# Kernel tuning notes

Measured on AMD Instinct MI355X. Metric: run time of the kernel, lower is better.

The kernel has to match this reference:

```python
import jax, jax.numpy as jnp
import numpy as np

M, N, P, T = 8000, 63, 64, 5


def setup_inputs() -> dict:
    key = jax.random.key(0)
    ks = jax.random.split(key, 19)
    sn = (1.0 / N) ** 0.5
    sp = (1.0 / P) ** 0.5
    f32 = jnp.float32
    return {
        "A": jax.random.normal(ks[0], (1, M, N), f32),
        "b": jax.random.normal(ks[1], (1, M), f32),
        "c": jax.random.normal(ks[2], (1, N), f32),
        "theta1r": sn * jax.random.normal(ks[3], (P, N + 1), f32),
        "theta1c": sn * jax.random.normal(ks[4], (P, N + 1), f32),
        "theta2rr": sp * jax.random.normal(ks[5], (P, P), f32),
        "theta2rc": sp * jax.random.normal(ks[6], (P, P), f32),
        "theta2cr": sp * jax.random.normal(ks[7], (P, P), f32),
        "theta3rr": sp * jax.random.normal(ks[8], (P, P), f32),
        "theta3rc": sp * jax.random.normal(ks[9], (P, P), f32),
        "theta3cr": sp * jax.random.normal(ks[10], (P, P), f32),
        "theta4rr": sp * jax.random.normal(ks[11], (P,), f32),
        "theta4rc": sp * jax.random.normal(ks[12], (P,), f32),
        "theta4cr": sp * jax.random.normal(ks[13], (P,), f32),
        "theta6r": sp * jax.random.normal(ks[14], (P, P), f32),
        "theta6c": sp * jax.random.normal(ks[15], (P, P), f32),
        "theta7": sp * jax.random.normal(ks[16], (P, P), f32),
        "W8": 0.05 * jax.random.normal(ks[17], (2, 2 * P), f32),
        "b8": 0.05 * jax.random.normal(ks[18], (2,), f32),
        "z": 7,
    }


def reference(A, b, c, theta1r, theta1c, theta2rr, theta2rc, theta2cr,
              theta3rr, theta3rc, theta3cr, theta4rr, theta4rc, theta4cr,
              theta6r, theta6c, theta7, W8, b8, z):
    relu = jax.nn.relu
    m, n = A.shape[1], A.shape[2]
    p = theta1r.shape[0]
    # raw node features: row node v -> [A[v,:], b[v]]; column node m -> [c, 0]
    Fr_raw = jnp.concatenate([A[0], b[0][:, None]], axis=1)        # (m, n+1)
    fc_raw = jnp.concatenate([c[0], jnp.zeros((1,), A.dtype)])     # (n+1,)
    Fr = Fr_raw / jnp.linalg.norm(Fr_raw, axis=1, keepdims=True)   # f(v), v < m
    fc = fc_raw / jnp.linalg.norm(fc_raw)                          # f(m)
    # edge weights w(v,u) = f(v).f(u) are detached in the original (float(...data))
    Frd = jax.lax.stop_gradient(Fr)
    fcd = jax.lax.stop_gradient(fc)
    Wrr = Frd @ Frd.T                                              # (m, m)
    dg = jnp.diagonal(Wrr)
    srr_pos = relu(Wrr).sum(axis=1) - relu(dg)                     # sum over u != v
    srr_neg = relu(-Wrr).sum(axis=1) - relu(-dg)
    wrc = Frd @ fcd                                                # (m,) = w(v, m)
    # identity: sum_u relu(t4 * w_u) = relu(t4) * sum_u relu(w_u) + relu(-t4) * sum_u relu(-w_u)
    Srr = relu(theta4rr)[:, None] * srr_pos[None, :] + relu(-theta4rr)[:, None] * srr_neg[None, :]
    Src = relu(theta4rc)[:, None] * relu(wrc)[None, :] + relu(-theta4rc)[:, None] * relu(-wrc)[None, :]
    scr = relu(theta4cr) * relu(wrc).sum() + relu(-theta4cr) * relu(-wrc).sum()
    edge_r = theta3rr @ Srr + theta3rc @ Src                       # (p, m), constant over t
    edge_c = theta3cr @ scr                                        # (p,)
    fz = Fr[z]                                                     # z < m: row node feature
    t1r = theta1r @ fz                                             # (p,)
    t1c = theta1c @ fz
    # mu init (p, m+1) = [[Ab^T, c0^T]; 0]; split into row columns / column node
    mu_r0 = jnp.zeros((p, m), A.dtype).at[: n + 1].set(Fr_raw.T)
    mu_c0 = jnp.zeros((p,), A.dtype).at[: n + 1].set(fc_raw)

    def step(carry, _):
        mu_r, mu_c = carry
        # row nodes: term2rr uses old mu[:, v]; term2rc uses old mu[:, m]
        new_r = relu(t1r[:, None] + theta2rr @ mu_r + (theta2rc @ mu_c)[:, None] + edge_r)
        # column node updated last within a sweep -> sees updated row embeddings
        new_c = relu(t1c + theta2cr @ new_r.sum(axis=1) + edge_c)
        return (new_r, new_c), None

    (mu_r, mu_c), _ = jax.lax.scan(step, (mu_r0, mu_c0), None, length=T)
    term6 = theta6r @ mu_r.sum(axis=1) + theta6c @ mu_c            # (p,)
    term7 = theta7 @ mu_r[:, z]                                    # (p,)
    feat = jax.nn.sigmoid(jnp.concatenate([term6, term7]))         # (2p,)
    return (feat @ W8.T + b8)[None, :]                             # (1, 2)
```

## Files before the change

### kernel.cpp

```cpp
#include <hip/hip_runtime.h>
#include <math.h>

typedef __attribute__((ext_vector_type(8))) short short8;
typedef __attribute__((ext_vector_type(4))) float f32x4;

#define WS_SPART 0
#define WS_GPART 262144
#define WS_WPART 270336
#define WS_CPART 270592
#define WS_T1R   310592
#define WS_T1C   310656
#define WS_AL    310720
#define WS_BE    310784
#define WS_GA    310848
#define WS_DE    310912
#define WS_ECP   310976
#define WS_ECN   311040
#define WS_W     311104
#define WS_MUZ   311168
#define WS_WSUM  311232
#define WS_RNORM 311296
#define WS_R2H   319488
#define WS_R2L   321536
#define WS_E4    323584
#define WS_FH    355584
#define WS_FL    617728

__device__ __forceinline__ float waveReduceSum(float v) {
#pragma unroll
    for (int m = 32; m >= 1; m >>= 1) v += __shfl_xor(v, m, 64);
    return v;
}
__device__ __forceinline__ unsigned short f2bf(float f) {
    unsigned int u = __float_as_uint(f);
    unsigned int r = (u + 0x7fffu + ((u >> 16) & 1u)) >> 16;
    return (unsigned short)r;
}
__device__ __forceinline__ float bf2f(unsigned short h) {
    return __uint_as_float(((unsigned int)h) << 16);
}

__global__ __launch_bounds__(256) void k_fr(
    const float* __restrict__ A, const float* __restrict__ b, const float* __restrict__ c,
    const float* __restrict__ th1r, const float* __restrict__ th1c,
    const float* __restrict__ th2rr, const float* __restrict__ th2rc,
    const float* __restrict__ th3rr, const float* __restrict__ th3rc, const float* __restrict__ th3cr,
    const float* __restrict__ th4rr, const float* __restrict__ th4rc, const float* __restrict__ th4cr,
    const int* __restrict__ zp,
    unsigned short* __restrict__ Fh, unsigned short* __restrict__ Fl,
    unsigned short* __restrict__ R2H, unsigned short* __restrict__ R2L,
    float* __restrict__ ws)
{
    int tid = threadIdx.x, lane = tid & 63, wid = tid >> 6;

    if (blockIdx.x == 128) {
        __shared__ float fcraw[64], fz[64], sh4a[64], sh4b[64];
        int p = lane;
        int z = zp[0];
        float cv = (p < 63) ? c[p] : 0.f;
        fcraw[p] = cv;
        float av = (p < 63) ? A[z * 63 + p] : b[z];
        float s2 = waveReduceSum(av * av);
        fz[p] = av * rsqrtf(s2);
        __syncthreads();

        float t1 = 0.f, t2 = 0.f, w0 = 0.f;
#pragma unroll 8
        for (int k = 0; k < 64; k++) {
            t1 += th1r[p * 64 + k] * fz[k];
            t2 += th1c[p * 64 + k] * fz[k];
            w0 += th2rc[p * 64 + k] * fcraw[k];
        }
        ws[WS_T1R + p] = t1;
        ws[WS_T1C + p] = t2;
        ws[WS_W + p] = t1 + w0;

        sh4a[p] = th4rr[p];
        sh4b[p] = th4rc[p];
        __syncthreads();
        float a = 0.f, bb = 0.f, g = 0.f, d = 0.f;
#pragma unroll 8
        for (int k = 0; k < 64; k++) {
            float t4 = sh4a[k];
            a  += th3rr[p * 64 + k] * fmaxf(t4, 0.f);
            bb += th3rr[p * 64 + k] * fmaxf(-t4, 0.f);
            float t5 = sh4b[k];
            g  += th3rc[p * 64 + k] * fmaxf(t5, 0.f);
            d  += th3rc[p * 64 + k] * fmaxf(-t5, 0.f);
        }
        ws[WS_AL + p] = a; ws[WS_BE + p] = bb;
        ws[WS_GA + p] = g; ws[WS_DE + p] = d;
        __syncthreads();
        sh4a[p] = th4cr[p];
        __syncthreads();
        float e1 = 0.f, e2 = 0.f;
#pragma unroll 8
        for (int k = 0; k < 64; k++) {
            float t6 = sh4a[k];
            e1 += th3cr[p * 64 + k] * fmaxf(t6, 0.f);
            e2 += th3cr[p * 64 + k] * fmaxf(-t6, 0.f);
        }
        ws[WS_ECP + p] = e1; ws[WS_ECN + p] = e2;

#pragma unroll
        for (int i = 0; i < 16; i++) {
            int idx = tid * 16 + i;
            float f = th2rr[idx];
            unsigned short h = f2bf(f);
            R2H[idx] = h;
            R2L[idx] = f2bf(f - bf2f(h));
        }
        return;
    }

    __shared__ float gsh[64];
    __shared__ float wsh2[2];
    if (tid < 64) gsh[tid] = 0.f;
    if (tid < 2) wsh2[tid] = 0.f;
    __syncthreads();

    float cv = (lane < 63) ? c[lane] : 0.f;
    float cn2 = waveReduceSum(cv * cv);
    float fcnl = cv * rsqrtf(cn2);

    int gw = blockIdx.x * 4 + wid;
    float gl = 0.f, lp = 0.f, ln = 0.f;
    for (int r = gw; r < 8192; r += 512) {
        if (r < 8000) {
            float val = (lane < 63) ? A[r * 63 + lane] : b[r];
            float s2 = waveReduceSum(val * val);
            float f = val * rsqrtf(s2);
            unsigned short h = f2bf(f);
            Fh[r * 64 + lane] = h;
            Fl[r * 64 + lane] = f2bf(f - bf2f(h));
            gl += f;
            float w = waveReduceSum(f * fcnl);
            if (lane == 0) {
                ws[WS_RNORM + r] = sqrtf(s2);
                lp += fmaxf(w, 0.f); ln += fmaxf(-w, 0.f);
            }
        } else {
            Fh[r * 64 + lane] = 0;
            Fl[r * 64 + lane] = 0;
        }
    }
    atomicAdd(&gsh[lane], gl);
    if (lane == 0) { atomicAdd(&wsh2[0], lp); atomicAdd(&wsh2[1], ln); }
    __syncthreads();
    if (tid < 64) ws[WS_GPART + blockIdx.x * 64 + tid] = gsh[tid];
    if (tid == 64) ws[WS_WPART + blockIdx.x * 2 + 0] = wsh2[0];
    if (tid == 65) ws[WS_WPART + blockIdx.x * 2 + 1] = wsh2[1];
}

__global__ __launch_bounds__(256) void k_gram(
    const unsigned short* __restrict__ Fh, const unsigned short* __restrict__ Fl,
    float* __restrict__ ws)
{
    int tid = threadIdx.x, lane = tid & 63, wid = tid >> 6;
    int m = lane & 15, quad = lane >> 4;
    int vbase = blockIdx.x * 256 + wid * 64;

    short8 AH[8], AL[8];
#pragma unroll
    for (int pt = 0; pt < 4; pt++)
#pragma unroll
        for (int q = 0; q < 2; q++) {
            int off = (vbase + pt * 16 + m) * 64 + q * 32 + quad * 8;
            AH[pt * 2 + q] = *(const short8*)(Fh + off);
            AL[pt * 2 + q] = *(const short8*)(Fl + off);
        }
    float srr[16];
#pragma unroll
    for (int i = 0; i < 16; i++) srr[i] = 0.f;

    const int y = blockIdx.y;
    const int boff = m * 64 + quad * 8;
    short8 B0h[2], B0l[2], B1h[2], B1l[2];
#pragma unroll
    for (int q = 0; q < 2; q++) {
        B0h[q] = *(const short8*)(Fh + y * 16 * 64 + boff + q * 32);
        B0l[q] = *(const short8*)(Fl + y * 16 * 64 + boff + q * 32);
    }
#pragma unroll 1
    for (int ii = 0; ii < 8; ii++) {
        int tB1 = y + 64 * ii + 32;
#pragma unroll
        for (int q = 0; q < 2; q++) {
            B1h[q] = *(const short8*)(Fh + tB1 * 16 * 64 + boff + q * 32);
            B1l[q] = *(const short8*)(Fl + tB1 * 16 * 64 + boff + q * 32);
        }
#pragma unroll
        for (int pt = 0; pt < 4; pt++) {
            f32x4 a = {0.f, 0.f, 0.f, 0.f};
#pragma unroll
            for (int q = 0; q < 2; q++) {
                a = __builtin_amdgcn_mfma_f32_16x16x32_bf16(AH[pt*2+q], B0h[q], a, 0, 0, 0);
                a = __builtin_amdgcn_mfma_f32_16x16x32_bf16(AH[pt*2+q], B0l[q], a, 0, 0, 0);
                a = __builtin_amdgcn_mfma_f32_16x16x32_bf16(AL[pt*2+q], B0h[q], a, 0, 0, 0);
            }
#pragma unroll
            for (int r = 0; r < 4; r++) srr[pt*4+r] += fmaxf(a[r], 0.f);
        }
        if (ii < 7) {
            int tB0 = y + 64 * ii + 64;
#pragma unroll
            for (int q = 0; q < 2; q++) {
                B0h[q] = *(const short8*)(Fh + tB0 * 16 * 64 + boff + q * 32);
                B0l[q] = *(const short8*)(Fl + tB0 * 16 * 64 + boff + q * 32);
            }
        }
#pragma unroll
        for (int pt = 0; pt < 4; pt++) {
            f32x4 a = {0.f, 0.f, 0.f, 0.f};
#pragma unroll
            for (int q = 0; q < 2; q++) {
                a = __builtin_amdgcn_mfma_f32_16x16x32_bf16(AH[pt*2+q], B1h[q], a, 0, 0, 0);
                a = __builtin_amdgcn_mfma_f32_16x16x32_bf16(AH[pt*2+q], B1l[q], a, 0, 0, 0);
                a = __builtin_amdgcn_mfma_f32_16x16x32_bf16(AL[pt*2+q], B1h[q], a, 0, 0, 0);
            }
#pragma unroll
            for (int r = 0; r < 4; r++) srr[pt*4+r] += fmaxf(a[r], 0.f);
        }
    }
#pragma unroll
    for (int pt = 0; pt < 4; pt++)
#pragma unroll
        for (int r = 0; r < 4; r++) {
            float s = srr[pt * 4 + r];
#pragma unroll
            for (int mm = 8; mm >= 1; mm >>= 1) s += __shfl_xor(s, mm, 64);
            if (m == 0)
                ws[WS_SPART + y * 8192 + vbase + pt * 16 + quad * 4 + r] = s;
        }
}

__global__ __launch_bounds__(256) void k_e4(
    const float* __restrict__ c, float* __restrict__ ws,
    unsigned short* __restrict__ MH, unsigned short* __restrict__ ML)
{
    __shared__ float fcnS[64], gS[64], sprow[64], red[256];
    int tid = threadIdx.x, lane = tid & 63, wid = tid >> 6;

    float cv = (lane < 63) ? c[lane] : 0.f;
    float cn2 = waveReduceSum(cv * cv);
    if (wid == 0) fcnS[lane] = cv * rsqrtf(cn2);

    float gv = 0.f;
#pragma unroll 8
    for (int blk = wid * 32; blk < wid * 32 + 32; blk++)
        gv += ws[WS_GPART + blk * 64 + lane];
    red[tid] = gv;
    __syncthreads();
    if (tid < 64) gS[tid] = red[tid] + red[64 + tid] + red[128 + tid] + red[192 + tid];
    if (wid == 1) {
        float wp = ws[WS_WPART + lane * 2] + ws[WS_WPART + (lane + 64) * 2];
        wp = waveReduceSum(wp);
        if (lane == 0) ws[WS_WSUM] = wp;
    }
    if (wid == 2) {
        float wn = ws[WS_WPART + lane * 2 + 1] + ws[WS_WPART + (lane + 64) * 2 + 1];
        wn = waveReduceSum(wn);
        if (lane == 0) ws[WS_WSUM + 1] = wn;
    }
    int v0 = blockIdx.x * 64;
    float sv = 0.f;
#pragma unroll
    for (int y = wid * 8; y < wid * 8 + 8; y++)
        sv += ws[WS_SPART + y * 8192 + v0 + lane];
    __syncthreads();
    red[tid] = sv;
    __syncthreads();
    if (tid < 64) sprow[tid] = red[tid] + red[64 + tid] + red[128 + tid] + red[192 + tid];
    __syncthreads();

    for (int i2 = 0; i2 < 16; i2++) {
        int i = wid * 16 + i2;
        int v = v0 + i;
        unsigned short fh = MH[v * 64 + lane];
        unsigned short fl = ML[v * 64 + lane];
        float fr = bf2f(fh) + bf2f(fl);
        float dw = waveReduceSum(fr * fcnS[lane]);
        float dg = waveReduceSum(fr * gS[lane]);
        if (lane == 0) {
            float spv = sprow[i];
            float4 e;
            e.x = spv - 1.0f;
            e.y = spv - dg;
            e.z = fmaxf(dw, 0.f);
            e.w = fmaxf(-dw, 0.f);
            *(float4*)(ws + WS_E4 + v * 4) = e;
        }
        float rnv = ws[WS_RNORM + v];
        float x = fr * rnv;
        unsigned short h = f2bf(x);
        MH[v * 64 + lane] = h;
        ML[v * 64 + lane] = f2bf(x - bf2f(h));
    }
}

__global__ __launch_bounds__(256) void k_iter(
    const float* __restrict__ th2cr, const float* __restrict__ th2rc,
    const int* __restrict__ zp, float* __restrict__ ws,
    unsigned short* __restrict__ MH, unsigned short* __restrict__ ML,
    const unsigned short* __restrict__ R2H, const unsigned short* __restrict__ R2L,
    int t)
{
    __shared__ __align__(16) float wsh[64], alS[64], beS[64], gaS[64], deS[64];
    __shared__ float red[256], Ssh[64], ysh[64], colp[256];
    int tid = threadIdx.x, lane = tid & 63, wid = tid >> 6;
    int m = lane & 15, quad = lane >> 4;
    int v = (blockIdx.x * 4 + wid) * 16 + m;

    if (tid < 64) {
        alS[tid] = ws[WS_AL + tid]; beS[tid] = ws[WS_BE + tid];
        gaS[tid] = ws[WS_GA + tid]; deS[tid] = ws[WS_DE + tid];
    }
    if (t == 0) {
        if (tid >= 64 && tid < 128) wsh[tid - 64] = ws[WS_W + tid - 64];
        __syncthreads();
    } else {
        float s = 0.f;
        for (int blk = wid; blk < 125; blk += 4)
            s += ws[WS_CPART + (t - 1) * 8000 + blk * 64 + lane];
        red[tid] = s;
        __syncthreads();
        if (tid < 64) Ssh[tid] = red[tid] + red[64 + tid] + red[128 + tid] + red[192 + tid];
        __syncthreads();
        {
            int p = wid * 16 + m;
            float acc = 0.f;
            const float4* rowp = (const float4*)(th2cr + p * 64 + quad * 16);
#pragma unroll
            for (int kk = 0; kk < 4; kk++) {
                float4 r4 = rowp[kk];
                acc += r4.x * Ssh[quad * 16 + 4 * kk]     + r4.y * Ssh[quad * 16 + 4 * kk + 1]
                     + r4.z * Ssh[quad * 16 + 4 * kk + 2] + r4.w * Ssh[quad * 16 + 4 * kk + 3];
            }
            acc += __shfl_xor(acc, 16, 64);
            acc += __shfl_xor(acc, 32, 64);
            if (quad == 0)
                ysh[p] = fmaxf(acc + ws[WS_T1C + p] + ws[WS_WSUM] * ws[WS_ECP + p]
                               + ws[WS_WSUM + 1] * ws[WS_ECN + p], 0.f);
        }
        __syncthreads();
        {
            int p = wid * 16 + m;
            float acc = 0.f;
            const float4* rowp = (const float4*)(th2rc + p * 64 + quad * 16);
#pragma unroll
            for (int kk = 0; kk < 4; kk++) {
                float4 r4 = rowp[kk];
                acc += r4.x * ysh[quad * 16 + 4 * kk]     + r4.y * ysh[quad * 16 + 4 * kk + 1]
                     + r4.z * ysh[quad * 16 + 4 * kk + 2] + r4.w * ysh[quad * 16 + 4 * kk + 3];
            }
            acc += __shfl_xor(acc, 16, 64);
            acc += __shfl_xor(acc, 32, 64);
            if (quad == 0) wsh[p] = acc + ws[WS_T1R + p];
        }
        __syncthreads();
    }

    short8 RH[8], RL[8];
#pragma unroll
    for (int pt = 0; pt < 4; pt++)
#pragma unroll
        for (int q = 0; q < 2; q++) {
            int off = (pt * 16 + m) * 64 + q * 32 + quad * 8;
            RH[pt * 2 + q] = *(const short8*)(R2H + off);
            RL[pt * 2 + q] = *(const short8*)(R2L + off);
        }
    short8 BH[2], BL[2];
#pragma unroll
    for (int q = 0; q < 2; q++) {
        BH[q] = *(const short8*)(MH + v * 64 + q * 32 + quad * 8);
        BL[q] = *(const short8*)(ML + v * 64 + q * 32 + quad * 8);
    }
    float4 e = *(const float4*)(ws + WS_E4 + v * 4);
    int z = zp[0];

#pragma unroll
    for (int pt = 0; pt < 4; pt++) {
        f32x4 a = {0.f, 0.f, 0.f, 0.f};
#pragma unroll
        for (int q = 0; q < 2; q++) {
            a = __builtin_amdgcn_mfma_f32_16x16x32_bf16(RH[pt*2+q], BH[q], a, 0, 0, 0);
            a = __builtin_amdgcn_mfma_f32_16x16x32_bf16(RH[pt*2+q], BL[q], a, 0, 0, 0);
            a = __builtin_amdgcn_mfma_f32_16x16x32_bf16(RL[pt*2+q], BH[q], a, 0, 0, 0);
        }
        int pbase = pt * 16 + quad * 4;
        float4 w4 = *(const float4*)(wsh + pbase);
        float4 a4 = *(const float4*)(alS + pbase);
        float4 b4 = *(const float4*)(beS + pbase);
        float4 g4 = *(const float4*)(gaS + pbase);
        float4 d4 = *(const float4*)(deS + pbase);
        float v0 = fmaxf(a[0] + w4.x + a4.x*e.x + b4.x*e.y + g4.x*e.z + d4.x*e.w, 0.f);
        float v1 = fmaxf(a[1] + w4.y + a4.y*e.x + b4.y*e.y + g4.y*e.z + d4.y*e.w, 0.f);
        float v2 = fmaxf(a[2] + w4.z + a4.z*e.x + b4.z*e.y + g4.z*e.z + d4.z*e.w, 0.f);
        float v3 = fmaxf(a[3] + w4.w + a4.w*e.x + b4.w*e.y + g4.w*e.z + d4.w*e.w, 0.f);
        ushort4 h4, l4;
        h4.x = f2bf(v0); l4.x = f2bf(v0 - bf2f(h4.x));
        h4.y = f2bf(v1); l4.y = f2bf(v1 - bf2f(h4.y));
        h4.z = f2bf(v2); l4.z = f2bf(v2 - bf2f(h4.z));
        h4.w = f2bf(v3); l4.w = f2bf(v3 - bf2f(h4.w));
        *(ushort4*)(MH + v * 64 + pbase) = h4;
        *(ushort4*)(ML + v * 64 + pbase) = l4;
        float c0 = v0, c1 = v1, c2 = v2, c3 = v3;
#pragma unroll
        for (int mm = 1; mm < 16; mm <<= 1) {
            c0 += __shfl_xor(c0, mm, 64);
            c1 += __shfl_xor(c1, mm, 64);
            c2 += __shfl_xor(c2, mm, 64);
            c3 += __shfl_xor(c3, mm, 64);
        }
        if (m == 0) {
            colp[wid * 64 + pbase + 0] = c0;
            colp[wid * 64 + pbase + 1] = c1;
            colp[wid * 64 + pbase + 2] = c2;
            colp[wid * 64 + pbase + 3] = c3;
        }
        if (t == 4 && v == z) {
            float4 o; o.x = v0; o.y = v1; o.z = v2; o.w = v3;
            *(float4*)(ws + WS_MUZ + pbase) = o;
        }
    }
    __syncthreads();
    if (tid < 64)
        ws[WS_CPART + t * 8000 + blockIdx.x * 64 + tid] =
            colp[tid] + colp[64 + tid] + colp[128 + tid] + colp[192 + tid];
}

__global__ __launch_bounds__(256) void k_head(
    const float* __restrict__ th2cr,
    const float* __restrict__ th6r, const float* __restrict__ th6c, const float* __restrict__ th7,
    const float* __restrict__ W8, const float* __restrict__ b8,
    float* __restrict__ ws, float* __restrict__ out)
{
    int tid = threadIdx.x, lane = tid & 63, wid = tid >> 6;
    __shared__ float red[256], S[64], y[64], feat[128];
    float s = 0.f;
    for (int blk = wid; blk < 125; blk += 4)
        s += ws[WS_CPART + 4 * 8000 + blk * 64 + lane];
    red[tid] = s;
    __syncthreads();
    if (tid < 64) S[tid] = red[tid] + red[64 + tid] + red[128 + tid] + red[192 + tid];
    __syncthreads();
    int p = tid;
    if (p < 64) {
        float acc = ws[WS_T1C + p] + ws[WS_WSUM] * ws[WS_ECP + p]
                  + ws[WS_WSUM + 1] * ws[WS_ECN + p];
#pragma unroll 8
        for (int k = 0; k < 64; k++) acc += th2cr[p * 64 + k] * S[k];
        y[p] = fmaxf(acc, 0.f);
    }
    __syncthreads();
    if (p < 64) {
        float t6 = 0.f, t7 = 0.f;
#pragma unroll 8
        for (int k = 0; k < 64; k++) {
            t6 += th6r[p * 64 + k] * S[k] + th6c[p * 64 + k] * y[k];
            t7 += th7[p * 64 + k] * ws[WS_MUZ + k];
        }
        feat[p] = 1.f / (1.f + expf(-t6));
        feat[64 + p] = 1.f / (1.f + expf(-t7));
    }
    __syncthreads();
    if (p < 2) {
        float o = b8[p];
        for (int i = 0; i < 128; i++) o += W8[p * 128 + i] * feat[i];
        out[p] = o;
    }
}

extern "C" void kernel_launch(void* const* d_in, const int* in_sizes, int n_in,
                              void* d_out, int out_size, void* d_ws, size_t ws_size,
                              hipStream_t stream) {
    (void)in_sizes; (void)n_in; (void)out_size; (void)ws_size;
    const float* A     = (const float*)d_in[0];
    const float* b     = (const float*)d_in[1];
    const float* c     = (const float*)d_in[2];
    const float* th1r  = (const float*)d_in[3];
    const float* th1c  = (const float*)d_in[4];
    const float* th2rr = (const float*)d_in[5];
    const float* th2rc = (const float*)d_in[6];
    const float* th2cr = (const float*)d_in[7];
    const float* th3rr = (const float*)d_in[8];
    const float* th3rc = (const float*)d_in[9];
    const float* th3cr = (const float*)d_in[10];
    const float* th4rr = (const float*)d_in[11];
    const float* th4rc = (const float*)d_in[12];
    const float* th4cr = (const float*)d_in[13];
    const float* th6r  = (const float*)d_in[14];
    const float* th6c  = (const float*)d_in[15];
    const float* th7   = (const float*)d_in[16];
    const float* W8    = (const float*)d_in[17];
    const float* b8    = (const float*)d_in[18];
    const int*   zp    = (const int*)d_in[19];
    float* ws  = (float*)d_ws;
    float* out = (float*)d_out;
    unsigned short* Fh  = (unsigned short*)(ws + WS_FH);
    unsigned short* Fl  = (unsigned short*)(ws + WS_FL);
    unsigned short* R2H = (unsigned short*)(ws + WS_R2H);
    unsigned short* R2L = (unsigned short*)(ws + WS_R2L);

    k_fr<<<129, 256, 0, stream>>>(A, b, c, th1r, th1c, th2rr, th2rc, th3rr, th3rc,
                                  th3cr, th4rr, th4rc, th4cr, zp, Fh, Fl, R2H, R2L, ws);
    k_gram<<<dim3(32, 32), 256, 0, stream>>>(Fh, Fl, ws);
    k_e4<<<125, 256, 0, stream>>>(c, ws, Fh, Fl);
    for (int t = 0; t < 5; t++)
        k_iter<<<125, 256, 0, stream>>>(th2cr, th2rc, zp, ws, Fh, Fl, R2H, R2L, t);
    k_head<<<1, 256, 0, stream>>>(th2cr, th6r, th6c, th7, W8, b8, ws, out);
}
```

Before: 238.1 us.

## Fuse e4, iterations and head into one persistent kernel with grid barrier

Result: slower. 266.5 us (+11.9%).

```diff
diff --git a/kernel.cpp b/kernel.cpp
--- a/kernel.cpp
+++ b/kernel.cpp
@@ -4,27 +4,28 @@
 typedef __attribute__((ext_vector_type(8))) short short8;
 typedef __attribute__((ext_vector_type(4))) float f32x4;
 
+#define NREC 125
+
 #define WS_SPART 0
 #define WS_GPART 262144
-#define WS_WPART 270336
-#define WS_CPART 270592
-#define WS_T1R   310592
-#define WS_T1C   310656
-#define WS_AL    310720
-#define WS_BE    310784
-#define WS_GA    310848
-#define WS_DE    310912
-#define WS_ECP   310976
-#define WS_ECN   311040
-#define WS_W     311104
-#define WS_MUZ   311168
-#define WS_WSUM  311232
-#define WS_RNORM 311296
-#define WS_R2H   319488
-#define WS_R2L   321536
-#define WS_E4    323584
-#define WS_FH    355584
-#define WS_FL    617728
+#define WS_WPART 294912
+#define WS_CPART 295936
+#define WS_T1R   335936
+#define WS_T1C   336000
+#define WS_AL    336064
+#define WS_BE    336128
+#define WS_GA    336192
+#define WS_DE    336256
+#define WS_ECP   336320
+#define WS_ECN   336384
+#define WS_W     336448
+#define WS_MUZ   336512
+#define WS_BAR   336576
+#define WS_RNORM 336640
+#define WS_R2H   344832
+#define WS_R2L   346880
+#define WS_FH    348928
+#define WS_FL    611072
 
 __device__ __forceinline__ float waveReduceSum(float v) {
 #pragma unroll
@@ -38,6 +39,25 @@
 }
 __device__ __forceinline__ float bf2f(unsigned short h) {
     return __uint_as_float(((unsigned int)h) << 16);
+}
+
+__device__ __forceinline__ void gridBarrier(float* ws) {
+    __syncthreads();
+    if (threadIdx.x == 0) {
+        __threadfence();
+        unsigned* bar = (unsigned*)(ws + WS_BAR);
+        unsigned gen = __hip_atomic_load(&bar[0], __ATOMIC_ACQUIRE, __HIP_MEMORY_SCOPE_AGENT);
+        unsigned prev = __hip_atomic_fetch_add(&bar[1], 1u, __ATOMIC_ACQ_REL, __HIP_MEMORY_SCOPE_AGENT);
+        if (prev == NREC - 1) {
+            __hip_atomic_store(&bar[1], 0u, __ATOMIC_RELAXED, __HIP_MEMORY_SCOPE_AGENT);
+            __hip_atomic_store(&bar[0], gen + 1u, __ATOMIC_RELEASE, __HIP_MEMORY_SCOPE_AGENT);
+        } else {
+            while (__hip_atomic_load(&bar[0], __ATOMIC_ACQUIRE, __HIP_MEMORY_SCOPE_AGENT) == gen)
+                __builtin_amdgcn_s_sleep(8);
+        }
+        __threadfence();
+    }
+    __syncthreads();
 }
 
 __global__ __launch_bounds__(256) void k_fr(
@@ -53,10 +73,11 @@
 {
     int tid = threadIdx.x, lane = tid & 63, wid = tid >> 6;
 
-    if (blockIdx.x == 128) {
+    if (blockIdx.x == 512) {
         __shared__ float fcraw[64], fz[64], sh4a[64], sh4b[64];
         int p = lane;
         int z = zp[0];
+        if (tid < 4) ws[WS_BAR + tid] = 0.f;
         float cv = (p < 63) ? c[p] : 0.f;
         fcraw[p] = cv;
         float av = (p < 63) ? A[z * 63 + p] : b[z];
@@ -123,9 +144,11 @@
     float cn2 = waveReduceSum(cv * cv);
     float fcnl = cv * rsqrtf(cn2);
 
-    int gw = blockIdx.x * 4 + wid;
+    int r0 = blockIdx.x * 16 + wid * 4;
     float gl = 0.f, lp = 0.f, ln = 0.f;
-    for (int r = gw; r < 8192; r += 512) {
+#pragma unroll
+    for (int i = 0; i < 4; i++) {
+        int r = r0 + i;
         if (r < 8000) {
             float val = (lane < 63) ? A[r * 63 + lane] : b[r];
             float s2 = waveReduceSum(val * val);
@@ -152,26 +175,40 @@
     if (tid == 65) ws[WS_WPART + blockIdx.x * 2 + 1] = wsh2[1];
 }
 
-__global__ __launch_bounds__(256) void k_gram(
+#define GRAM_STEP(Bh_, Bl_)                                                         \
+    _Pragma("unroll")                                                               \
+    for (int pt = 0; pt < 8; pt++) {                                                \
+        f32x4 a = {0.f, 0.f, 0.f, 0.f};                                             \
+        _Pragma("unroll")                                                           \
+        for (int q = 0; q < 2; q++) {                                               \
+            a = __builtin_amdgcn_mfma_f32_16x16x32_bf16(AH[pt*2+q], Bh_[q], a, 0, 0, 0); \
+            a = __builtin_amdgcn_mfma_f32_16x16x32_bf16(AH[pt*2+q], Bl_[q], a, 0, 0, 0); \
+            a = __builtin_amdgcn_mfma_f32_16x16x32_bf16(AL[pt*2+q], Bh_[q], a, 0, 0, 0); \
+        }                                                                           \
+        _Pragma("unroll")                                                           \
+        for (int r = 0; r < 4; r++) srr[pt*4+r] += fmaxf(a[r], 0.f);                \
+    }
+
+__global__ __launch_bounds__(256, 2) void k_gram(
     const unsigned short* __restrict__ Fh, const unsigned short* __restrict__ Fl,
     float* __restrict__ ws)
 {
     int tid = threadIdx.x, lane = tid & 63, wid = tid >> 6;
     int m = lane & 15, quad = lane >> 4;
-    int vbase = blockIdx.x * 256 + wid * 64;
-
-    short8 AH[8], AL[8];
-#pragma unroll
-    for (int pt = 0; pt < 4; pt++)
+    int vbase = blockIdx.x * 512 + wid * 128;
+
+    short8 AH[16], AL[16];
+#pragma unroll
+    for (int pt = 0; pt < 8; pt++)
 #pragma unroll
         for (int q = 0; q < 2; q++) {
             int off = (vbase + pt * 16 + m) * 64 + q * 32 + quad * 8;
             AH[pt * 2 + q] = *(const short8*)(Fh + off);
             AL[pt * 2 + q] = *(const short8*)(Fl + off);
         }
-    float srr[16];
-#pragma unroll
-    for (int i = 0; i < 16; i++) srr[i] = 0.f;
+    float srr[32];
+#pragma unroll
+    for (int i = 0; i < 32; i++) srr[i] = 0.f;
 
     const int y = blockIdx.y;
     const int boff = m * 64 + quad * 8;
@@ -182,48 +219,26 @@
         B0l[q] = *(const short8*)(Fl + y * 16 * 64 + boff + q * 32);
     }
 #pragma unroll 1
-    for (int ii = 0; ii < 8; ii++) {
-        int tB1 = y + 64 * ii + 32;
+    for (int k2 = 0; k2 < 8; k2++) {
+        int jB1 = y + 32 * (2 * k2 + 1);
 #pragma unroll
         for (int q = 0; q < 2; q++) {
-            B1h[q] = *(const short8*)(Fh + tB1 * 16 * 64 + boff + q * 32);
-            B1l[q] = *(const short8*)(Fl + tB1 * 16 * 64 + boff + q * 32);
-        }
-#pragma unroll
-        for (int pt = 0; pt < 4; pt++) {
-            f32x4 a = {0.f, 0.f, 0.f, 0.f};
+            B1h[q] = *(const short8*)(Fh + jB1 * 16 * 64 + boff + q * 32);
+            B1l[q] = *(const short8*)(Fl + jB1 * 16 * 64 + boff + q * 32);
+        }
+        GRAM_STEP(B0h, B0l)
+        if (k2 < 7) {
+            int jB0 = y + 32 * (2 * k2 + 2);
 #pragma unroll
             for (int q = 0; q < 2; q++) {
-                a = __builtin_amdgcn_mfma_f32_16x16x32_bf16(AH[pt*2+q], B0h[q], a, 0, 0, 0);
-                a = __builtin_amdgcn_mfma_f32_16x16x32_bf16(AH[pt*2+q], B0l[q], a, 0, 0, 0);
-                a = __builtin_amdgcn_mfma_f32_16x16x32_bf16(AL[pt*2+q], B0h[q], a, 0, 0, 0);
-            }
-#pragma unroll
-            for (int r = 0; r < 4; r++) srr[pt*4+r] += fmaxf(a[r], 0.f);
-        }
-        if (ii < 7) {
-            int tB0 = y + 64 * ii + 64;
-#pragma unroll
-            for (int q = 0; q < 2; q++) {
-                B0h[q] = *(const short8*)(Fh + tB0 * 16 * 64 + boff + q * 32);
-                B0l[q] = *(const short8*)(Fl + tB0 * 16 * 64 + boff + q * 32);
-            }
-        }
-#pragma unroll
-        for (int pt = 0; pt < 4; pt++) {
-            f32x4 a = {0.f, 0.f, 0.f, 0.f};
-#pragma unroll
-            for (int q = 0; q < 2; q++) {
-                a = __builtin_amdgcn_mfma_f32_16x16x32_bf16(AH[pt*2+q], B1h[q], a, 0, 0, 0);
-                a = __builtin_amdgcn_mfma_f32_16x16x32_bf16(AH[pt*2+q], B1l[q], a, 0, 0, 0);
-                a = __builtin_amdgcn_mfma_f32_16x16x32_bf16(AL[pt*2+q], B1h[q], a, 0, 0, 0);
-            }
-#pragma unroll
-            for (int r = 0; r < 4; r++) srr[pt*4+r] += fmaxf(a[r], 0.f);
-        }
-    }
-#pragma unroll
-    for (int pt = 0; pt < 4; pt++)
+                B0h[q] = *(const short8*)(Fh + jB0 * 16 * 64 + boff + q * 32);
+                B0l[q] = *(const short8*)(Fl + jB0 * 16 * 64 + boff + q * 32);
+            }
+        }
+        GRAM_STEP(B1h, B1l)
+    }
+#pragma unroll
+    for (int pt = 0; pt < 8; pt++)
 #pragma unroll
         for (int r = 0; r < 4; r++) {
             float s = srr[pt * 4 + r];
@@ -234,40 +249,63 @@
         }
 }
 
-__global__ __launch_bounds__(256) void k_e4(
-    const float* __restrict__ c, float* __restrict__ ws,
-    unsigned short* __restrict__ MH, unsigned short* __restrict__ ML)
+__global__ __launch_bounds__(256) void k_rec(
+    const float* __restrict__ c,
+    const float* __restrict__ th2cr, const float* __restrict__ th2rc,
+    const float* __restrict__ th6r, const float* __restrict__ th6c,
+    const float* __restrict__ th7, const float* __restrict__ W8,
+    const float* __restrict__ b8, const int* __restrict__ zp,
+    float* __restrict__ ws, unsigned short* __restrict__ MH,
+    unsigned short* __restrict__ ML,
+    const unsigned short* __restrict__ R2H, const unsigned short* __restrict__ R2L,
+    float* __restrict__ out)
 {
     __shared__ float fcnS[64], gS[64], sprow[64], red[256];
+    __shared__ __align__(16) float e4sh[256];
+    __shared__ __align__(16) float wshS[64], alS[64], beS[64], gaS[64], deS[64];
+    __shared__ float t1rS[64], t1cS[64], ecpS[64], ecnS[64];
+    __shared__ float SshS[64], yshS[64], colp[256], wsumS[2], feat[128];
+
     int tid = threadIdx.x, lane = tid & 63, wid = tid >> 6;
-
-    float cv = (lane < 63) ? c[lane] : 0.f;
-    float cn2 = waveReduceSum(cv * cv);
-    if (wid == 0) fcnS[lane] = cv * rsqrtf(cn2);
-
+    int m = lane & 15, quad = lane >> 4;
+    int vblk = blockIdx.x * 64;
+    int vloc = wid * 16 + m;
+    int v = vblk + vloc;
+    int z = zp[0];
+
+    if (wid == 0) {
+        float cv = (lane < 63) ? c[lane] : 0.f;
+        float cn2 = waveReduceSum(cv * cv);
+        fcnS[lane] = cv * rsqrtf(cn2);
+        wshS[lane] = ws[WS_W + lane];
+        t1rS[lane] = ws[WS_T1R + lane];
+        t1cS[lane] = ws[WS_T1C + lane];
+    } else if (wid == 1) {
+        alS[lane] = ws[WS_AL + lane]; beS[lane] = ws[WS_BE + lane];
+        float wp = 0.f;
+#pragma unroll
+        for (int k = 0; k < 8; k++) wp += ws[WS_WPART + (lane + 64 * k) * 2];
+        wp = waveReduceSum(wp);
+        if (lane == 0) wsumS[0] = wp;
+    } else if (wid == 2) {
+        gaS[lane] = ws[WS_GA + lane]; deS[lane] = ws[WS_DE + lane];
+        float wn = 0.f;
+#pragma unroll
+        for (int k = 0; k < 8; k++) wn += ws[WS_WPART + (lane + 64 * k) * 2 + 1];
+        wn = waveReduceSum(wn);
+        if (lane == 0) wsumS[1] = wn;
+    } else {
+        ecpS[lane] = ws[WS_ECP + lane]; ecnS[lane] = ws[WS_ECN + lane];
+    }
     float gv = 0.f;
-#pragma unroll 8
-    for (int blk = wid * 32; blk < wid * 32 + 32; blk++)
-        gv += ws[WS_GPART + blk * 64 + lane];
+    for (int bb = 0; bb < 128; bb++) gv += ws[WS_GPART + (wid * 128 + bb) * 64 + lane];
     red[tid] = gv;
     __syncthreads();
     if (tid < 64) gS[tid] = red[tid] + red[64 + tid] + red[128 + tid] + red[192 + tid];
-    if (wid == 1) {
-        float wp = ws[WS_WPART + lane * 2] + ws[WS_WPART + (lane + 64) * 2];
-        wp = waveReduceSum(wp);
-        if (lane == 0) ws[WS_WSUM] = wp;
-    }
-    if (wid == 2) {
-        float wn = ws[WS_WPART + lane * 2 + 1] + ws[WS_WPART + (lane + 64) * 2 + 1];
-        wn = waveReduceSum(wn);
-        if (lane == 0) ws[WS_WSUM + 1] = wn;
-    }
-    int v0 = blockIdx.x * 64;
+    __syncthreads();
     float sv = 0.f;
 #pragma unroll
-    for (int y = wid * 8; y < wid * 8 + 8; y++)
-        sv += ws[WS_SPART + y * 8192 + v0 + lane];
-    __syncthreads();
+    for (int y = wid * 8; y < wid * 8 + 8; y++) sv += ws[WS_SPART + y * 8192 + vblk + lane];
     red[tid] = sv;
     __syncthreads();
     if (tid < 64) sprow[tid] = red[tid] + red[64 + tid] + red[128 + tid] + red[192 + tid];
@@ -275,89 +313,21 @@
 
     for (int i2 = 0; i2 < 16; i2++) {
         int i = wid * 16 + i2;
-        int v = v0 + i;
-        unsigned short fh = MH[v * 64 + lane];
-        unsigned short fl = ML[v * 64 + lane];
-        float fr = bf2f(fh) + bf2f(fl);
+        int vr = vblk + i;
+        float fr = bf2f(MH[vr * 64 + lane]) + bf2f(ML[vr * 64 + lane]);
         float dw = waveReduceSum(fr * fcnS[lane]);
         float dg = waveReduceSum(fr * gS[lane]);
         if (lane == 0) {
             float spv = sprow[i];
-            float4 e;
-            e.x = spv - 1.0f;
-            e.y = spv - dg;
-            e.z = fmaxf(dw, 0.f);
-            e.w = fmaxf(-dw, 0.f);
-            *(float4*)(ws + WS_E4 + v * 4) = e;
-        }
-        float rnv = ws[WS_RNORM + v];
-        float x = fr * rnv;
+            e4sh[i * 4 + 0] = spv - 1.0f;
+            e4sh[i * 4 + 1] = spv - dg;
+            e4sh[i * 4 + 2] = fmaxf(dw, 0.f);
+            e4sh[i * 4 + 3] = fmaxf(-dw, 0.f);
+        }
+        float x = fr * ws[WS_RNORM + vr];
         unsigned short h = f2bf(x);
-        MH[v * 64 + lane] = h;
-        ML[v * 64 + lane] = f2bf(x - bf2f(h));
-    }
-}
-
-__global__ __launch_bounds__(256) void k_iter(
-    const float* __restrict__ th2cr, const float* __restrict__ th2rc,
-    const int* __restrict__ zp, float* __restrict__ ws,
-    unsigned short* __restrict__ MH, unsigned short* __restrict__ ML,
-    const unsigned short* __restrict__ R2H, const unsigned short* __restrict__ R2L,
-    int t)
-{
-    __shared__ __align__(16) float wsh[64], alS[64], beS[64], gaS[64], deS[64];
-    __shared__ float red[256], Ssh[64], ysh[64], colp[256];
-    int tid = threadIdx.x, lane = tid & 63, wid = tid >> 6;
-    int m = lane & 15, quad = lane >> 4;
-    int v = (blockIdx.x * 4 + wid) * 16 + m;
-
-    if (tid < 64) {
-        alS[tid] = ws[WS_AL + tid]; beS[tid] = ws[WS_BE + tid];
-        gaS[tid] = ws[WS_GA + tid]; deS[tid] = ws[WS_DE + tid];
-    }
-    if (t == 0) {
-        if (tid >= 64 && tid < 128) wsh[tid - 64] = ws[WS_W + tid - 64];
-        __syncthreads();
-    } else {
-        float s = 0.f;
-        for (int blk = wid; blk < 125; blk += 4)
-            s += ws[WS_CPART + (t - 1) * 8000 + blk * 64 + lane];
-        red[tid] = s;
-        __syncthreads();
-        if (tid < 64) Ssh[tid] = red[tid] + red[64 + tid] + red[128 + tid] + red[192 + tid];
-        __syncthreads();
-        {
-            int p = wid * 16 + m;
-            float acc = 0.f;
-            const float4* rowp = (const float4*)(th2cr + p * 64 + quad * 16);
-#pragma unroll
-            for (int kk = 0; kk < 4; kk++) {
-                float4 r4 = rowp[kk];
-                acc += r4.x * Ssh[quad * 16 + 4 * kk]     + r4.y * Ssh[quad * 16 + 4 * kk + 1]
-                     + r4.z * Ssh[quad * 16 + 4 * kk + 2] + r4.w * Ssh[quad * 16 + 4 * kk + 3];
-            }
-            acc += __shfl_xor(acc, 16, 64);
-            acc += __shfl_xor(acc, 32, 64);
-            if (quad == 0)
-                ysh[p] = fmaxf(acc + ws[WS_T1C + p] + ws[WS_WSUM] * ws[WS_ECP + p]
-                               + ws[WS_WSUM + 1] * ws[WS_ECN + p], 0.f);
-        }
-        __syncthreads();
-        {
-            int p = wid * 16 + m;
-            float acc = 0.f;
-            const float4* rowp = (const float4*)(th2rc + p * 64 + quad * 16);
-#pragma unroll
-            for (int kk = 0; kk < 4; kk++) {
-                float4 r4 = rowp[kk];
-                acc += r4.x * ysh[quad * 16 + 4 * kk]     + r4.y * ysh[quad * 16 + 4 * kk + 1]
-                     + r4.z * ysh[quad * 16 + 4 * kk + 2] + r4.w * ysh[quad * 16 + 4 * kk + 3];
-            }
-            acc += __shfl_xor(acc, 16, 64);
-            acc += __shfl_xor(acc, 32, 64);
-            if (quad == 0) wsh[p] = acc + ws[WS_T1R + p];
-        }
-        __syncthreads();
+        MH[vr * 64 + lane] = h;
+        ML[vr * 64 + lane] = f2bf(x - bf2f(h));
     }
 
     short8 RH[8], RL[8];
@@ -369,105 +339,141 @@
             RH[pt * 2 + q] = *(const short8*)(R2H + off);
             RL[pt * 2 + q] = *(const short8*)(R2L + off);
         }
-    short8 BH[2], BL[2];
-#pragma unroll
-    for (int q = 0; q < 2; q++) {
-        BH[q] = *(const short8*)(MH + v * 64 + q * 32 + quad * 8);
-        BL[q] = *(const short8*)(ML + v * 64 + q * 32 + quad * 8);
-    }
-    float4 e = *(const float4*)(ws + WS_E4 + v * 4);
-    int z = zp[0];
-
-#pragma unroll
-    for (int pt = 0; pt < 4; pt++) {
-        f32x4 a = {0.f, 0.f, 0.f, 0.f};
+    __syncthreads();
+    float4 e = *(const float4*)(e4sh + vloc * 4);
+
+    for (int t = 0; t < 5; t++) {
+        if (t > 0) {
+            float s = 0.f;
+            for (int blk = wid; blk < NREC; blk += 4)
+                s += ws[WS_CPART + (t - 1) * 8000 + blk * 64 + lane];
+            red[tid] = s;
+            __syncthreads();
+            if (tid < 64) SshS[tid] = red[tid] + red[64 + tid] + red[128 + tid] + red[192 + tid];
+            __syncthreads();
+            {
+                int p = wid * 16 + m;
+                float acc = 0.f;
+                const float4* rowp = (const float4*)(th2cr + p * 64 + quad * 16);
+#pragma unroll
+                for (int kk = 0; kk < 4; kk++) {
+                    float4 r4 = rowp[kk];
+                    acc += r4.x * SshS[quad * 16 + 4 * kk]     + r4.y * SshS[quad * 16 + 4 * kk + 1]
+                         + r4.z * SshS[quad * 16 + 4 * kk + 2] + r4.w * SshS[quad * 16 + 4 * kk + 3];
+                }
+                acc += __shfl_xor(acc, 16, 64);
+                acc += __shfl_xor(acc, 32, 64);
+                if (quad == 0)
+                    yshS[p] = fmaxf(acc + t1cS[p] + wsumS[0] * ecpS[p] + wsumS[1] * ecnS[p], 0.f);
+            }
+            __syncthreads();
+            {
+                int p = wid * 16 + m;
+                float acc = 0.f;
+                const float4* rowp = (const float4*)(th2rc + p * 64 + quad * 16);
+#pragma unroll
+                for (int kk = 0; kk < 4; kk++) {
+                    float4 r4 = rowp[kk];
+                    acc += r4.x * yshS[quad * 16 + 4 * kk]     + r4.y * yshS[quad * 16 + 4 * kk + 1]
+                         + r4.z * yshS[quad * 16 + 4 * kk + 2] + r4.w * yshS[quad * 16 + 4 * kk + 3];
+                }
+                acc += __shfl_xor(acc, 16, 64);
+                acc += __shfl_xor(acc, 32, 64);
+                if (quad == 0) wshS[p] = acc + t1rS[p];
+            }
+            __syncthreads();
+        }
+
+        short8 BH[2], BL[2];
 #pragma unroll
         for (int q = 0; q < 2; q++) {
-            a = __builtin_amdgcn_mfma_f32_16x16x32_bf16(RH[pt*2+q], BH[q], a, 0, 0, 0);
-            a = __builtin_amdgcn_mfma_f32_16x16x32_bf16(RH[pt*2+q], BL[q], a, 0, 0, 0);
-            a = __builtin_amdgcn_mfma_f32_16x16x32_bf16(RL[pt*2+q], BH[q], a, 0, 0, 0);
-        }
-        int pbase = pt * 16 + quad * 4;
-        float4 w4 = *(const float4*)(wsh + pbase);
-        float4 a4 = *(const float4*)(alS + pbase);
-        float4 b4 = *(const float4*)(beS + pbase);
-        float4 g4 = *(const float4*)(gaS + pbase);
-        float4 d4 = *(const float4*)(deS + pbase);
-        float v0 = fmaxf(a[0] + w4.x + a4.x*e.x + b4.x*e.y + g4.x*e.z + d4.x*e.w, 0.f);
-        float v1 = fmaxf(a[1] + w4.y + a4.y*e.x + b4.y*e.y + g4.y*e.z + d4.y*e.w, 0.f);
-        float v2 = fmaxf(a[2] + w4.z + a4.z*e.x + b4.z*e.y + g4.z*e.z + d4.z*e.w, 0.f);
-        float v3 = fmaxf(a[3] + w4.w + a4.w*e.x + b4.w*e.y + g4.w*e.z + d4.w*e.w, 0.f);
-        ushort4 h4, l4;
-        h4.x = f2bf(v0); l4.x = f2bf(v0 - bf2f(h4.x));
-        h4.y = f2bf(v1); l4.y = f2bf(v1 - bf2f(h4.y));
-        h4.z = f2bf(v2); l4.z = f2bf(v2 - bf2f(h4.z));
-        h4.w = f2bf(v3); l4.w = f2bf(v3 - bf2f(h4.w));
-        *(ushort4*)(MH + v * 64 + pbase) = h4;
-        *(ushort4*)(ML + v * 64 + pbase) = l4;
-        float c0 = v0, c1 = v1, c2 = v2, c3 = v3;
-#pragma unroll
-        for (int mm = 1; mm < 16; mm <<= 1) {
-            c0 += __shfl_xor(c0, mm, 64);
-            c1 += __shfl_xor(c1, mm, 64);
-            c2 += __shfl_xor(c2, mm, 64);
-            c3 += __shfl_xor(c3, mm, 64);
-        }
-        if (m == 0) {
-            colp[wid * 64 + pbase + 0] = c0;
-            colp[wid * 64 + pbase + 1] = c1;
-            colp[wid * 64 + pbase + 2] = c2;
-            colp[wid * 64 + pbase + 3] = c3;
-        }
-        if (t == 4 && v == z) {
-            float4 o; o.x = v0; o.y = v1; o.z = v2; o.w = v3;
-            *(float4*)(ws + WS_MUZ + pbase) = o;
-        }
-    }
-    __syncthreads();
-    if (tid < 64)
-        ws[WS_CPART + t * 8000 + blockIdx.x * 64 + tid] =
-            colp[tid] + colp[64 + tid] + colp[128 + tid] + colp[192 + tid];
-}
-
-__global__ __launch_bounds__(256) void k_head(
-    const float* __restrict__ th2cr,
-    const float* __restrict__ th6r, const float* __restrict__ th6c, const float* __restrict__ th7,
-    const float* __restrict__ W8, const float* __restrict__ b8,
-    float* __restrict__ ws, float* __restrict__ out)
-{
-    int tid = threadIdx.x, lane = tid & 63, wid = tid >> 6;
-    __shared__ float red[256], S[64], y[64], feat[128];
-    float s = 0.f;
-    for (int blk = wid; blk < 125; blk += 4)
-        s += ws[WS_CPART + 4 * 8000 + blk * 64 + lane];
-    red[tid] = s;
-    __syncthreads();
-    if (tid < 64) S[tid] = red[tid] + red[64 + tid] + red[128 + tid] + red[192 + tid];
-    __syncthreads();
-    int p = tid;
-    if (p < 64) {
-        float acc = ws[WS_T1C + p] + ws[WS_WSUM] * ws[WS_ECP + p]
-                  + ws[WS_WSUM + 1] * ws[WS_ECN + p];
+            BH[q] = *(const short8*)(MH + v * 64 + q * 32 + quad * 8);
+            BL[q] = *(const short8*)(ML + v * 64 + q * 32 + quad * 8);
+        }
+#pragma unroll
+        for (int pt = 0; pt < 4; pt++) {
+            f32x4 a = {0.f, 0.f, 0.f, 0.f};
+#pragma unroll
+            for (int q = 0; q < 2; q++) {
+                a = __builtin_amdgcn_mfma_f32_16x16x32_bf16(RH[pt*2+q], BH[q], a, 0, 0, 0);
+                a = __builtin_amdgcn_mfma_f32_16x16x32_bf16(RH[pt*2+q], BL[q], a, 0, 0, 0);
+                a = __builtin_amdgcn_mfma_f32_16x16x32_bf16(RL[pt*2+q], BH[q], a, 0, 0, 0);
+            }
+            int pbase = pt * 16 + quad * 4;
+            float4 w4 = *(const float4*)(wshS + pbase);
+            float4 a4 = *(const float4*)(alS + pbase);
+            float4 b4 = *(const float4*)(beS + pbase);
+            float4 g4 = *(const float4*)(gaS + pbase);
+            float4 d4 = *(const float4*)(deS + pbase);
+            float u0 = fmaxf(a[0] + w4.x + a4.x*e.x + b4.x*e.y + g4.x*e.z + d4.x*e.w, 0.f);
+            float u1 = fmaxf(a[1] + w4.y + a4.y*e.x + b4.y*e.y + g4.y*e.z + d4.y*e.w, 0.f);
+            float u2 = fmaxf(a[2] + w4.z + a4.z*e.x + b4.z*e.y + g4.z*e.z + d4.z*e.w, 0.f);
+            float u3 = fmaxf(a[3] + w4.w + a4.w*e.x + b4.w*e.y + g4.w*e.z + d4.w*e.w, 0.f);
+            ushort4 h4, l4;
+            h4.x = f2bf(u0); l4.x = f2bf(u0 - bf2f(h4.x));
+            h4.y = f2bf(u1); l4.y = f2bf(u1 - bf2f(h4.y));
+            h4.z = f2bf(u2); l4.z = f2bf(u2 - bf2f(h4.z));
+            h4.w = f2bf(u3); l4.w = f2bf(u3 - bf2f(h4.w));
+            *(ushort4*)(MH + v * 64 + pbase) = h4;
+            *(ushort4*)(ML + v * 64 + pbase) = l4;
+            float c0 = u0, c1 = u1, c2 = u2, c3 = u3;
+#pragma unroll
+            for (int mm = 1; mm < 16; mm <<= 1) {
+                c0 += __shfl_xor(c0, mm, 64);
+                c1 += __shfl_xor(c1, mm, 64);
+                c2 += __shfl_xor(c2, mm, 64);
+                c3 += __shfl_xor(c3, mm, 64);
+            }
+            if (m == 0) {
+                colp[wid * 64 + pbase + 0] = c0;
+                colp[wid * 64 + pbase + 1] = c1;
+                colp[wid * 64 + pbase + 2] = c2;
+                colp[wid * 64 + pbase + 3] = c3;
+            }
+            if (t == 4 && v == z) {
+                float4 o; o.x = u0; o.y = u1; o.z = u2; o.w = u3;
+                *(float4*)(ws + WS_MUZ + pbase) = o;
+            }
+        }
+        __syncthreads();
+        if (tid < 64)
+            ws[WS_CPART + t * 8000 + blockIdx.x * 64 + tid] =
+                colp[tid] + colp[64 + tid] + colp[128 + tid] + colp[192 + tid];
+        gridBarrier(ws);
+    }
+
+    if (blockIdx.x == 0) {
+        float s = 0.f;
+        for (int blk = wid; blk < NREC; blk += 4)
+            s += ws[WS_CPART + 4 * 8000 + blk * 64 + lane];
+        red[tid] = s;
+        __syncthreads();
+        if (tid < 64) SshS[tid] = red[tid] + red[64 + tid] + red[128 + tid] + red[192 + tid];
+        __syncthreads();
+        int p = tid;
+        if (p < 64) {
+            float acc = t1cS[p] + wsumS[0] * ecpS[p] + wsumS[1] * ecnS[p];
 #pragma unroll 8
-        for (int k = 0; k < 64; k++) acc += th2cr[p * 64 + k] * S[k];
-        y[p] = fmaxf(acc, 0.f);
-    }
-    __syncthreads();
-    if (p < 64) {
-        float t6 = 0.f, t7 = 0.f;
+            for (int k = 0; k < 64; k++) acc += th2cr[p * 64 + k] * SshS[k];
+            yshS[p] = fmaxf(acc, 0.f);
+        }
+        __syncthreads();
+        if (p < 64) {
+            float t6 = 0.f, t7 = 0.f;
 #pragma unroll 8
-        for (int k = 0; k < 64; k++) {
-            t6 += th6r[p * 64 + k] * S[k] + th6c[p * 64 + k] * y[k];
-            t7 += th7[p * 64 + k] * ws[WS_MUZ + k];
-        }
-        feat[p] = 1.f / (1.f + expf(-t6));
-        feat[64 + p] = 1.f / (1.f + expf(-t7));
-    }
-    __syncthreads();
-    if (p < 2) {
-        float o = b8[p];
-        for (int i = 0; i < 128; i++) o += W8[p * 128 + i] * feat[i];
-        out[p] = o;
+            for (int k = 0; k < 64; k++) {
+                t6 += th6r[p * 64 + k] * SshS[k] + th6c[p * 64 + k] * yshS[k];
+                t7 += th7[p * 64 + k] * ws[WS_MUZ + k];
+            }
+            feat[p] = 1.f / (1.f + expf(-t6));
+            feat[64 + p] = 1.f / (1.f + expf(-t7));
+        }
+        __syncthreads();
+        if (p < 2) {
+            float o = b8[p];
+            for (int i = 0; i < 128; i++) o += W8[p * 128 + i] * feat[i];
+            out[p] = o;
+        }
     }
 }
 
@@ -502,11 +508,9 @@
     unsigned short* R2H = (unsigned short*)(ws + WS_R2H);
     unsigned short* R2L = (unsigned short*)(ws + WS_R2L);
 
-    k_fr<<<129, 256, 0, stream>>>(A, b, c, th1r, th1c, th2rr, th2rc, th3rr, th3rc,
+    k_fr<<<513, 256, 0, stream>>>(A, b, c, th1r, th1c, th2rr, th2rc, th3rr, th3rc,
                                   th3cr, th4rr, th4rc, th4cr, zp, Fh, Fl, R2H, R2L, ws);
-    k_gram<<<dim3(32, 32), 256, 0, stream>>>(Fh, Fl, ws);
-    k_e4<<<125, 256, 0, stream>>>(c, ws, Fh, Fl);
-    for (int t = 0; t < 5; t++)
-        k_iter<<<125, 256, 0, stream>>>(th2cr, th2rc, zp, ws, Fh, Fl, R2H, R2L, t);
-    k_head<<<1, 256, 0, stream>>>(th2cr, th6r, th6c, th7, W8, b8, ws, out);
-}
+    k_gram<<<dim3(16, 32), 256, 0, stream>>>(Fh, Fl, ws);
+    k_rec<<<NREC, 256, 0, stream>>>(c, th2cr, th2rc, th6r, th6c, th7, W8, b8, zp,
+                                    ws, Fh, Fl, R2H, R2L, out);
+}
```
